# Kernel tuning notes

Measured on AMD Instinct MI355X. Metric: run time of the kernel, lower is better.

## Reference

```python
import jax, jax.numpy as jnp
import numpy as np

# ---- architecture constants (from init_kwargs / arch_args) ----
IN_BITS, IN_FRAC, BITS_PER_STREAM = 8, 4, 2
N_STREAMS = IN_BITS // BITS_PER_STREAM          # 4
W_BITS, BITS_PER_SLICE = 8, 2
N_SLICES = W_BITS // BITS_PER_SLICE             # 4
ADC_BITS = 5
ADC_MAX = 2.0 ** ADC_BITS - 1.0                 # 31
SUBARRAY_SIZE = 128
IC, OC, K, STRIDE, PAD = 64, 64, 3, 1, 1
F_TOTAL = IC * K * K                            # 576 unfolded features
N_SUB = (F_TOTAL + SUBARRAY_SIZE - 1) // SUBARRAY_SIZE  # 5 subarrays
CHUNK = -(-F_TOTAL // N_SUB)                    # 116, matches torch.chunk sizes


def bit_stream(x):
    """VectorizedInputBitStreaming.forward: fixed-point quantize + two's complement + bit-serial split."""
    int_bits = IN_BITS - IN_FRAC - 1
    max_val = 2.0 ** int_bits - 2.0 ** (-IN_FRAC)
    q = jnp.round(jnp.clip(x, -(2.0 ** int_bits), max_val) * (2 ** IN_FRAC)).astype(jnp.int32)
    q = jnp.where(q < 0, (1 << IN_BITS) + q, q)  # two's complement encode
    shifts = jnp.arange(0, IN_BITS, BITS_PER_STREAM, dtype=jnp.int32)
    return ((q[..., None] >> shifts) & ((1 << BITS_PER_STREAM) - 1)).astype(jnp.float32)


def bit_slice(w):
    """VectorizedWeightBitSlicing.forward: pos/neg split, normalize by max abs, integer bit-slice."""
    wp = jnp.maximum(w, 0.0)
    wn = jnp.maximum(-w, 0.0)
    max_abs = jnp.maximum(wp.max(), wn.max())
    max_abs = jnp.where(max_abs > 0, max_abs, 1.0)
    mv = 2 ** W_BITS - 1
    pi = jnp.round(wp / max_abs * mv).astype(jnp.int32)
    ni = jnp.round(wn / max_abs * mv).astype(jnp.int32)
    shifts = jnp.arange(0, W_BITS, BITS_PER_SLICE, dtype=jnp.int32)
    mask = (1 << BITS_PER_SLICE) - 1
    pos = ((pi[..., None] >> shifts) & mask).astype(jnp.float32)
    neg = ((ni[..., None] >> shifts) & mask).astype(jnp.float32)
    return pos, neg, max_abs


def adc(x):
    """Nbit_ADC simulated: uniform round + clip to [0, 2^adc_bits - 1]."""
    return jnp.clip(jnp.round(x), 0.0, ADC_MAX)


def _forward(inputs, weight):
    # unfold -> (B, IC*K*K, H', W') with (c, kh, kw)-major feature ordering like F.unfold
    patches = jax.lax.conv_general_dilated_patches(
        inputs, (K, K), (STRIDE, STRIDE), [(PAD, PAD), (PAD, PAD)])
    B, F, H, W = patches.shape
    P = H * W
    patches = patches.reshape(B, F, P)

    streams = bit_stream(patches)                     # (B, F, P, S)
    pos_sl, neg_sl, norm = bit_slice(weight)
    pos_m = pos_sl.reshape(OC, F, N_SLICES)           # (O, F, T)
    neg_m = neg_sl.reshape(OC, F, N_SLICES)

    # zero-pad feature dim to N_SUB*CHUNK and reshape into subarray chunks
    pad = N_SUB * CHUNK - F
    streams = jnp.pad(streams, ((0, 0), (0, pad), (0, 0), (0, 0))).reshape(B, N_SUB, CHUNK, P, N_STREAMS)
    pos_m = jnp.pad(pos_m, ((0, 0), (0, pad), (0, 0))).reshape(OC, N_SUB, CHUNK, N_SLICES)
    neg_m = jnp.pad(neg_m, ((0, 0), (0, pad), (0, 0))).reshape(OC, N_SUB, CHUNK, N_SLICES)

    # per-subarray analog MAC: (c, b, o, p, s, t)
    pos_r = jnp.einsum('bcfps,ocft->cbopst', streams, pos_m)
    neg_r = jnp.einsum('bcfps,ocft->cbopst', streams, neg_m)

    # ADC quantize, then weight by 2^(stream*bits) * 2^(slice*bits), sum over s,t and subarrays c
    scale = (2.0 ** (jnp.arange(N_STREAMS) * BITS_PER_STREAM))[:, None] * \
            (2.0 ** (jnp.arange(N_SLICES) * BITS_PER_SLICE))[None, :]
    diff = jnp.einsum('cbopst,st->bop', adc(pos_r) - adc(neg_r), scale)

    out = diff * norm / (2.0 ** IN_BITS - 1.0)
    return out.reshape(B, OC, H, W), jnp.float32(0.0)


def setup_inputs() -> dict:
    key = jax.random.key(0)
    k1, k2 = jax.random.split(key)
    inputs = jax.random.normal(k1, (4, IC, 32, 32), dtype=jnp.float32)
    # kaiming_normal_-like init
    weight = jax.random.normal(k2, (OC, IC, K, K), dtype=jnp.float32) * (2.0 / (IC * K * K)) ** 0.5
    return {"inputs": inputs, "weight": weight}


def reference(inputs, weight):
    return _forward(inputs, weight)
```

## Files before the change

kernel.cpp:

```cpp
#include <hip/hip_runtime.h>
#include <stdint.h>


typedef int v4i __attribute__((ext_vector_type(4)));
typedef unsigned int v4u __attribute__((ext_vector_type(4)));

#define WS_NORM   0
#define WS_QIMG   1024
#define WS_AQ     263168
#define WS_BP     2884608
#define WS_BN     2925568
#define WS_TOTAL  2966528

__global__ __launch_bounds__(256) void k_prep1(
    const float* __restrict__ in, const float* __restrict__ w,
    unsigned char* __restrict__ qimg, unsigned int* __restrict__ nrm,
    float* __restrict__ out_scalar)
{
  int bid = blockIdx.x, tid = threadIdx.x;
  if (bid == 0 && tid == 0) out_scalar[0] = 0.0f;
  if (bid < 1024) {
    int idx = bid * 256 + tid;
    float x = in[idx];
    x = fminf(fmaxf(x, -8.0f), 7.9375f);
    int q = (int)rintf(x * 16.0f);
    qimg[idx] = (unsigned char)(q & 255);
  } else {
    int idx = (bid - 1024) * 256 + tid;
    float a = fabsf(w[idx]);
    #pragma unroll
    for (int off = 32; off > 0; off >>= 1)
      a = fmaxf(a, __shfl_down(a, off, 64));
    if ((tid & 63) == 0)
      atomicMax(nrm, __float_as_uint(a));
  }
}

__global__ __launch_bounds__(256) void k_prep2(
    const float* __restrict__ w, const unsigned char* __restrict__ qimg,
    const unsigned int* __restrict__ nrmu,
    unsigned char* __restrict__ Aq, unsigned char* __restrict__ Bp,
    unsigned char* __restrict__ Bn)
{
  int bid = blockIdx.x, tid = threadIdx.x;
  if (bid < 160) {
    float norm = __uint_as_float(*nrmu);
    if (!(norm > 0.0f)) norm = 1.0f;
    int idx = bid * 256 + tid;
    int c   = idx >> 13;
    int rem = idx & 8191;
    int o   = rem >> 7;
    int k   = rem & 127;
    int csize = (c == 4) ? 112 : 116;
    unsigned char pb = 0, nb = 0;
    if (k < csize) {
      float wv = w[o * 576 + c * 116 + k];
      float wp = fmaxf(wv, 0.0f);
      float wn = fmaxf(-wv, 0.0f);
      pb = (unsigned char)(int)rintf(wp / norm * 255.0f);
      nb = (unsigned char)(int)rintf(wn / norm * 255.0f);
    }
    int addr = (c * 2 + (k >> 6)) * 4096 + o * 64 + (k & 63);
    Bp[addr] = pb;
    Bn[addr] = nb;
  } else {
    int widx = (bid - 160) * 256 + tid;
    int m  = widx / 160;
    int kw = widx - m * 160;
    int b = m >> 10, p = m & 1023;
    int y = p >> 5, x = p & 31;
    unsigned int pack = 0;
    #pragma unroll
    for (int i = 0; i < 4; ++i) {
      int k = kw * 4 + i;
      int c = k >> 7;
      int j = k & 127;
      int csize = (c == 4) ? 112 : 116;
      unsigned int bv = 0;
      if (j < csize) {
        int f  = c * 116 + j;
        int ic = f / 9;
        int r9 = f - ic * 9;
        int kh = r9 / 3;
        int k2 = r9 - kh * 3;
        int iy = y + kh - 1, ix = x + k2 - 1;
        if (iy >= 0 && iy < 32 && ix >= 0 && ix < 32)
          bv = qimg[((b * 64 + ic) * 32 + iy) * 32 + ix];
      }
      pack |= bv << (8 * i);
    }
    ((unsigned int*)Aq)[widx] = pack;
  }
}

__device__ __forceinline__ v4i bits2(v4u w, int s) {
  v4u r = (w >> (unsigned)(2 * s)) & 0x03030303u;
  return (v4i)r;
}

__global__ __launch_bounds__(256) void k_main(
    const unsigned char* __restrict__ Aq,
    const unsigned char* __restrict__ Bp,
    const unsigned char* __restrict__ Bn,
    const unsigned int* __restrict__ nrmu,
    float* __restrict__ out)
{
  int lane  = threadIdx.x & 63;
  int wave  = threadIdx.x >> 6;
  int mtile = blockIdx.x >> 2;
  int otile = blockIdx.x & 3;
  int r16  = lane & 15;
  int kgrp = lane >> 4;
  int m = mtile * 64 + wave * 16 + r16;
  int o = otile * 16 + r16;

  const unsigned char* ap  = Aq + m * 640 + kgrp * 16;
  const unsigned char* bpp = Bp + o * 64 + kgrp * 16;
  const unsigned char* bnp = Bn + o * 64 + kgrp * 16;

  v4i outacc = {0, 0, 0, 0};

  #pragma unroll
  for (int c = 0; c < 5; ++c) {
    v4u a0 = *(const v4u*)(ap + c * 128);
    v4u a1 = *(const v4u*)(ap + c * 128 + 64);
    v4u p0 = *(const v4u*)(bpp + (c * 2 + 0) * 4096);
    v4u p1 = *(const v4u*)(bpp + (c * 2 + 1) * 4096);
    v4u n0 = *(const v4u*)(bnp + (c * 2 + 0) * 4096);
    v4u n1 = *(const v4u*)(bnp + (c * 2 + 1) * 4096);

    v4i btp0[4], btp1[4], btn0[4], btn1[4];
    #pragma unroll
    for (int t = 0; t < 4; ++t) {
      btp0[t] = bits2(p0, t); btp1[t] = bits2(p1, t);
      btn0[t] = bits2(n0, t); btn1[t] = bits2(n1, t);
    }

    #pragma unroll
    for (int s = 0; s < 4; ++s) {
      v4i as0 = bits2(a0, s), as1 = bits2(a1, s);
      #pragma unroll
      for (int t = 0; t < 4; ++t) {
        v4i z = {0, 0, 0, 0};
        v4i pacc = __builtin_amdgcn_mfma_i32_16x16x64_i8(as0, btp0[t], z, 0, 0, 0);
        pacc     = __builtin_amdgcn_mfma_i32_16x16x64_i8(as1, btp1[t], pacc, 0, 0, 0);
        v4i nacc = __builtin_amdgcn_mfma_i32_16x16x64_i8(as0, btn0[t], z, 0, 0, 0);
        nacc     = __builtin_amdgcn_mfma_i32_16x16x64_i8(as1, btn1[t], nacc, 0, 0, 0);
        int sh = 2 * (s + t);
        #pragma unroll
        for (int r = 0; r < 4; ++r) {
          int d = (pacc[r] < 31 ? pacc[r] : 31) - (nacc[r] < 31 ? nacc[r] : 31);
          outacc[r] += d << sh;
        }
      }
    }
  }

  float norm = __uint_as_float(*nrmu);
  if (!(norm > 0.0f)) norm = 1.0f;
  int oc = otile * 16 + r16;
  #pragma unroll
  for (int r = 0; r < 4; ++r) {
    int mo = mtile * 64 + wave * 16 + kgrp * 4 + r;
    int b = mo >> 10, p = mo & 1023;
    out[(b * 64 + oc) * 1024 + p] = ((float)outacc[r] * norm) / 255.0f;
  }
}

extern "C" void kernel_launch(void* const* d_in, const int* in_sizes, int n_in,
                              void* d_out, int out_size, void* d_ws, size_t ws_size,
                              hipStream_t stream) {
  const float* inp = (const float*)d_in[0];
  const float* wgt = (const float*)d_in[1];
  float* out = (float*)d_out;
  unsigned char* ws = (unsigned char*)d_ws;

  unsigned int*  nrm  = (unsigned int*)(ws + WS_NORM);
  unsigned char* qimg = ws + WS_QIMG;
  unsigned char* Aq   = ws + WS_AQ;
  unsigned char* Bp   = ws + WS_BP;
  unsigned char* Bn   = ws + WS_BN;

  hipMemsetAsync(nrm, 0, 4, stream);
  k_prep1<<<1168, 256, 0, stream>>>(inp, wgt, qimg, nrm, out + 262144);
  k_prep2<<<2720, 256, 0, stream>>>(wgt, qimg, nrm, Aq, Bp, Bn);
  k_main <<<256, 256, 0, stream>>>(Aq, Bp, Bn, nrm, out);
}
```

Before: 81.81 us.

## Fuse prep kernels, build weight slices in shared memory, drop memset and atomics

Merges input quantization into the im2col packing so the quantized image buffer disappears. Weight max-abs now goes to per-block partials instead of an atomic. Weight quantization moves into the main kernel, where each block builds its pos/neg tiles in LDS. This cuts the launches from a memset plus three kernels to two, trading redundant weight quantization per block and extra LDS setup for less launch and global-memory traffic. Integer divides are replaced with multiply-shift tricks.

```diff
diff --git a/kernel.cpp b/kernel.cpp
--- a/kernel.cpp
+++ b/kernel.cpp
@@ -5,91 +5,60 @@
 typedef int v4i __attribute__((ext_vector_type(4)));
 typedef unsigned int v4u __attribute__((ext_vector_type(4)));
 
-#define WS_NORM   0
-#define WS_QIMG   1024
-#define WS_AQ     263168
-#define WS_BP     2884608
-#define WS_BN     2925568
-#define WS_TOTAL  2966528
+#define WS_PART   0
+#define WS_AQ     1024
+#define N_PART    144
 
-__global__ __launch_bounds__(256) void k_prep1(
+__device__ __forceinline__ unsigned char quant_in(float x) {
+  x = fminf(fmaxf(x, -8.0f), 7.9375f);
+  int q = (int)rintf(x * 16.0f);
+  return (unsigned char)(q & 255);
+}
+
+__global__ __launch_bounds__(256) void k_prep(
     const float* __restrict__ in, const float* __restrict__ w,
-    unsigned char* __restrict__ qimg, unsigned int* __restrict__ nrm,
+    unsigned char* __restrict__ Aq, float* __restrict__ part,
     float* __restrict__ out_scalar)
 {
   int bid = blockIdx.x, tid = threadIdx.x;
   if (bid == 0 && tid == 0) out_scalar[0] = 0.0f;
-  if (bid < 1024) {
-    int idx = bid * 256 + tid;
-    float x = in[idx];
-    x = fminf(fmaxf(x, -8.0f), 7.9375f);
-    int q = (int)rintf(x * 16.0f);
-    qimg[idx] = (unsigned char)(q & 255);
-  } else {
-    int idx = (bid - 1024) * 256 + tid;
-    float a = fabsf(w[idx]);
-    #pragma unroll
-    for (int off = 32; off > 0; off >>= 1)
-      a = fmaxf(a, __shfl_down(a, off, 64));
-    if ((tid & 63) == 0)
-      atomicMax(nrm, __float_as_uint(a));
-  }
-}
-
-__global__ __launch_bounds__(256) void k_prep2(
-    const float* __restrict__ w, const unsigned char* __restrict__ qimg,
-    const unsigned int* __restrict__ nrmu,
-    unsigned char* __restrict__ Aq, unsigned char* __restrict__ Bp,
-    unsigned char* __restrict__ Bn)
-{
-  int bid = blockIdx.x, tid = threadIdx.x;
-  if (bid < 160) {
-    float norm = __uint_as_float(*nrmu);
-    if (!(norm > 0.0f)) norm = 1.0f;
-    int idx = bid * 256 + tid;
-    int c   = idx >> 13;
-    int rem = idx & 8191;
-    int o   = rem >> 7;
-    int k   = rem & 127;
-    int csize = (c == 4) ? 112 : 116;
-    unsigned char pb = 0, nb = 0;
-    if (k < csize) {
-      float wv = w[o * 576 + c * 116 + k];
-      float wp = fmaxf(wv, 0.0f);
-      float wn = fmaxf(-wv, 0.0f);
-      pb = (unsigned char)(int)rintf(wp / norm * 255.0f);
-      nb = (unsigned char)(int)rintf(wn / norm * 255.0f);
-    }
-    int addr = (c * 2 + (k >> 6)) * 4096 + o * 64 + (k & 63);
-    Bp[addr] = pb;
-    Bn[addr] = nb;
-  } else {
-    int widx = (bid - 160) * 256 + tid;
-    int m  = widx / 160;
-    int kw = widx - m * 160;
+  if (bid < 2560) {
+    unsigned int widx = bid * 256 + tid;
+    unsigned int m  = ((widx >> 5) * 52429u) >> 18;
+    unsigned int kw = widx - m * 160;
     int b = m >> 10, p = m & 1023;
     int y = p >> 5, x = p & 31;
     unsigned int pack = 0;
     #pragma unroll
     for (int i = 0; i < 4; ++i) {
-      int k = kw * 4 + i;
-      int c = k >> 7;
-      int j = k & 127;
-      int csize = (c == 4) ? 112 : 116;
+      unsigned int k = kw * 4 + i;
+      unsigned int c = k >> 7;
+      unsigned int j = k & 127;
+      unsigned int csize = (c == 4) ? 112 : 116;
       unsigned int bv = 0;
       if (j < csize) {
-        int f  = c * 116 + j;
-        int ic = f / 9;
-        int r9 = f - ic * 9;
-        int kh = r9 / 3;
-        int k2 = r9 - kh * 3;
-        int iy = y + kh - 1, ix = x + k2 - 1;
+        unsigned int f  = c * 116 + j;
+        unsigned int ic = (f * 7282u) >> 16;
+        unsigned int r9 = f - ic * 9;
+        unsigned int dy = (r9 * 11u) >> 5;
+        unsigned int dx = r9 - dy * 3;
+        int iy = y + (int)dy - 1, ix = x + (int)dx - 1;
         if (iy >= 0 && iy < 32 && ix >= 0 && ix < 32)
-          bv = qimg[((b * 64 + ic) * 32 + iy) * 32 + ix];
+          bv = quant_in(in[((b * 64 + ic) * 32 + iy) * 32 + ix]);
       }
       pack |= bv << (8 * i);
     }
     ((unsigned int*)Aq)[widx] = pack;
+  } else {
+    int t = (bid - 2560) * 256 + tid;
+    const float4 wv = ((const float4*)w)[t];
+    float a = fmaxf(fmaxf(fabsf(wv.x), fabsf(wv.y)),
+                    fmaxf(fabsf(wv.z), fabsf(wv.w)));
+    #pragma unroll
+    for (int off = 32; off > 0; off >>= 1)
+      a = fmaxf(a, __shfl_down(a, off, 64));
+    if ((tid & 63) == 0)
+      part[(bid - 2560) * 4 + (tid >> 6)] = a;
   }
 }
 
@@ -98,25 +67,59 @@
   return (v4i)r;
 }
 
+#define BROW 656
+
 __global__ __launch_bounds__(256) void k_main(
-    const unsigned char* __restrict__ Aq,
-    const unsigned char* __restrict__ Bp,
-    const unsigned char* __restrict__ Bn,
-    const unsigned int* __restrict__ nrmu,
-    float* __restrict__ out)
+    const unsigned char* __restrict__ Aq, const float* __restrict__ w,
+    const float* __restrict__ part, float* __restrict__ out)
 {
-  int lane  = threadIdx.x & 63;
-  int wave  = threadIdx.x >> 6;
+  __shared__ unsigned char Bl[2][16][BROW];
+  __shared__ float s_norm;
+
+  int tid   = threadIdx.x;
+  int lane  = tid & 63;
+  int wave  = tid >> 6;
   int mtile = blockIdx.x >> 2;
   int otile = blockIdx.x & 3;
+
+  #pragma unroll
+  for (int i = 0; i < 21; ++i) {
+    int d = i * 256 + tid;
+    if (d < 2 * 16 * BROW / 4) ((unsigned int*)Bl)[d] = 0u;
+  }
+  if (wave == 0) {
+    float a = part[lane];
+    a = fmaxf(a, part[lane + 64]);
+    if (lane < 16) a = fmaxf(a, part[lane + 128]);
+    #pragma unroll
+    for (int off = 32; off > 0; off >>= 1)
+      a = fmaxf(a, __shfl_down(a, off, 64));
+    if (lane == 0) s_norm = (a > 0.0f) ? a : 1.0f;
+  }
+  __syncthreads();
+
+  float norm = s_norm;
+  float sc = 255.0f / norm;
+  #pragma unroll
+  for (int it = 0; it < 36; ++it) {
+    int idx = it * 256 + tid;
+    unsigned int ol = (((unsigned)idx >> 6) * 7282u) >> 16;
+    unsigned int f  = idx - ol * 576;
+    float wv = w[(otile * 16 + ol) * 576 + f];
+    unsigned int c = (f * 565u) >> 16;
+    unsigned int j = f - c * 116;
+    int kpos = c * 128 + j;
+    Bl[0][ol][kpos] = (unsigned char)(int)rintf(fmaxf(wv, 0.0f) * sc);
+    Bl[1][ol][kpos] = (unsigned char)(int)rintf(fmaxf(-wv, 0.0f) * sc);
+  }
+  __syncthreads();
+
   int r16  = lane & 15;
   int kgrp = lane >> 4;
   int m = mtile * 64 + wave * 16 + r16;
-  int o = otile * 16 + r16;
-
-  const unsigned char* ap  = Aq + m * 640 + kgrp * 16;
-  const unsigned char* bpp = Bp + o * 64 + kgrp * 16;
-  const unsigned char* bnp = Bn + o * 64 + kgrp * 16;
+  const unsigned char* ap = Aq + m * 640 + kgrp * 16;
+  const unsigned char* bp = &Bl[0][r16][kgrp * 16];
+  const unsigned char* bn = &Bl[1][r16][kgrp * 16];
 
   v4i outacc = {0, 0, 0, 0};
 
@@ -124,10 +127,10 @@
   for (int c = 0; c < 5; ++c) {
     v4u a0 = *(const v4u*)(ap + c * 128);
     v4u a1 = *(const v4u*)(ap + c * 128 + 64);
-    v4u p0 = *(const v4u*)(bpp + (c * 2 + 0) * 4096);
-    v4u p1 = *(const v4u*)(bpp + (c * 2 + 1) * 4096);
-    v4u n0 = *(const v4u*)(bnp + (c * 2 + 0) * 4096);
-    v4u n1 = *(const v4u*)(bnp + (c * 2 + 1) * 4096);
+    v4u p0 = *(const v4u*)(bp + c * 128);
+    v4u p1 = *(const v4u*)(bp + c * 128 + 64);
+    v4u n0 = *(const v4u*)(bn + c * 128);
+    v4u n1 = *(const v4u*)(bn + c * 128 + 64);
 
     v4i btp0[4], btp1[4], btn0[4], btn1[4];
     #pragma unroll
@@ -156,14 +159,13 @@
     }
   }
 
-  float norm = __uint_as_float(*nrmu);
-  if (!(norm > 0.0f)) norm = 1.0f;
+  float fsc = norm / 255.0f;
   int oc = otile * 16 + r16;
   #pragma unroll
   for (int r = 0; r < 4; ++r) {
     int mo = mtile * 64 + wave * 16 + kgrp * 4 + r;
     int b = mo >> 10, p = mo & 1023;
-    out[(b * 64 + oc) * 1024 + p] = ((float)outacc[r] * norm) / 255.0f;
+    out[(b * 64 + oc) * 1024 + p] = (float)outacc[r] * fsc;
   }
 }
 
@@ -175,14 +177,9 @@
   float* out = (float*)d_out;
   unsigned char* ws = (unsigned char*)d_ws;
 
-  unsigned int*  nrm  = (unsigned int*)(ws + WS_NORM);
-  unsigned char* qimg = ws + WS_QIMG;
+  float*         part = (float*)(ws + WS_PART);
   unsigned char* Aq   = ws + WS_AQ;
-  unsigned char* Bp   = ws + WS_BP;
-  unsigned char* Bn   = ws + WS_BN;
 
-  hipMemsetAsync(nrm, 0, 4, stream);
-  k_prep1<<<1168, 256, 0, stream>>>(inp, wgt, qimg, nrm, out + 262144);
-  k_prep2<<<2720, 256, 0, stream>>>(wgt, qimg, nrm, Aq, Bp, Bn);
-  k_main <<<256, 256, 0, stream>>>(Aq, Bp, Bn, nrm, out);
+  k_prep<<<2596, 256, 0, stream>>>(inp, wgt, Aq, part, out + 262144);
+  k_main<<<256, 256, 0, stream>>>(Aq, wgt, part, out);
 }
```

Measured after the change: 79.58 us. 2.7% less time.
